# Optimization experiments

Measured on AMD Instinct MI355X. Metric: run time of the kernel, lower is better.

Reference implementation:

```python
import jax, jax.numpy as jnp
import numpy as np

N_NODES = 100000
N_EDGES = 800000
IN_FEATS = 64
H_FEATS = 64
INTER = 64
NUM_CLASSES = 32
NEG_SLOPE = 0.01  # torch leaky_relu default


def setup_inputs() -> dict:
    key = jax.random.key(0)
    ks = jax.random.split(key, 16)
    inp = {
        "gate_type": jax.random.randint(ks[0], (N_NODES,), 0, IN_FEATS),
        "src": jax.random.randint(ks[1], (N_EDGES,), 0, N_NODES),
        "dst": jax.random.randint(ks[2], (N_EDGES,), 0, N_NODES),
        "src_idx": jax.random.uniform(ks[3], (N_EDGES,), dtype=jnp.float32),
        "dst_idx": jax.random.uniform(ks[4], (N_EDGES,), dtype=jnp.float32),
        "rev": jax.random.uniform(ks[5], (N_EDGES,), dtype=jnp.float32),
        "emb": jax.random.normal(ks[6], (IN_FEATS, IN_FEATS), dtype=jnp.float32) * 0.1,
        # 5 stacked QConv layers (in_feats == h_feats so shapes coincide)
        "W1": jax.random.normal(ks[7], (5, INTER, IN_FEATS + 3), dtype=jnp.float32) * 0.1,
        "W2": jax.random.normal(ks[8], (5, H_FEATS, IN_FEATS + INTER), dtype=jnp.float32) * 0.1,
        "b2": jnp.zeros((5, H_FEATS), dtype=jnp.float32),
        "Wl1": jax.random.normal(ks[9], (H_FEATS, H_FEATS), dtype=jnp.float32) * 0.1,
        "bl1": jnp.zeros((H_FEATS,), dtype=jnp.float32),
        "Wl2": jax.random.normal(ks[10], (NUM_CLASSES, H_FEATS), dtype=jnp.float32) * 0.1,
        "bl2": jnp.zeros((NUM_CLASSES,), dtype=jnp.float32),
    }
    return inp


def _leaky_relu(x):
    return jnp.where(x >= 0, x, NEG_SLOPE * x)


def reference(gate_type, src, dst, src_idx, dst_idx, rev,
              emb, W1, W2, b2, Wl1, bl1, Wl2, bl2):
    n = gate_type.shape[0]
    # edge feature w: [E, 3]
    w = jnp.stack([src_idx, dst_idx, rev], axis=1)
    # in-degree for mailbox mean (zero-degree nodes get h_N = 0, as in DGL)
    deg = jax.ops.segment_sum(jnp.ones((src.shape[0],), w.dtype), dst, num_segments=n)
    inv_deg = (1.0 / jnp.maximum(deg, 1.0))[:, None]  # [N, 1]

    h = emb[gate_type]  # [N, F] embedding lookup
    for i in range(5):
        m = jnp.concatenate([h[src], w], axis=1)          # [E, F+3] gather
        tmp = _leaky_relu(m @ W1[i].T)                     # [E, inter]
        h_N = jax.ops.segment_sum(tmp, dst, num_segments=n) * inv_deg  # mean mailbox
        h = jax.nn.relu(jnp.concatenate([h, h_N], axis=1) @ W2[i].T + b2[i])
    h = jax.nn.relu(h @ Wl1.T + bl1)
    return h @ Wl2.T + bl2  # [N, num_classes]
```

## Files before the change

kernel.cpp:

```cpp
#include <hip/hip_runtime.h>

#define NN 100000
#define NE 800000
#define NBLK 391
#define NBUCK 196
#define EPB 3125
#define BCAP 6144

typedef __attribute__((ext_vector_type(8))) short short8;
typedef __attribute__((ext_vector_type(4))) float f32x4;

__device__ __forceinline__ unsigned short f2b(float x) {
  unsigned int u = __float_as_uint(x);
  u = u + 0x7fffu + ((u >> 16) & 1u);
  return (unsigned short)(u >> 16);
}
__device__ __forceinline__ float b2f(unsigned short s) {
  return __uint_as_float(((unsigned int)s) << 16);
}


__global__ __launch_bounds__(256) void ehist(const int* __restrict__ dst,
                                             int* __restrict__ hp) {
  __shared__ int lh[NBUCK];
  int tid = threadIdx.x;
  if (tid < NBUCK) lh[tid] = 0;
  __syncthreads();
  int e0 = blockIdx.x * EPB;
  for (int i = tid; i < EPB; i += 256) atomicAdd(&lh[dst[e0 + i] >> 9], 1);
  __syncthreads();
  if (tid < NBUCK) hp[blockIdx.x * NBUCK + tid] = lh[tid];
}

__global__ void escan(int* __restrict__ hp, int* __restrict__ bucket_start) {
  __shared__ int ws[4];
  int b = threadIdx.x;
  int running = 0;
  if (b < NBUCK) {
    for (int blk = 0; blk < 256; ++blk) {
      int t = hp[blk * NBUCK + b];
      hp[blk * NBUCK + b] = running;
      running += t;
    }
  }
  int lane = b & 63, wv = b >> 6;
  int v = running;
#pragma unroll
  for (int off = 1; off < 64; off <<= 1) {
    int t = __shfl_up(v, off);
    if (lane >= off) v += t;
  }
  if (lane == 63) ws[wv] = v;
  __syncthreads();
  int wpre = 0;
  for (int j = 0; j < wv; ++j) wpre += ws[j];
  int excl = v + wpre - running;
  if (b <= NBUCK) bucket_start[b] = excl;
}

__global__ __launch_bounds__(256) void escatter(
    const int* __restrict__ dst, const int* __restrict__ hp,
    const int* __restrict__ bucket_start, unsigned int* __restrict__ ebkt) {
  __shared__ int cur[NBUCK];
  int tid = threadIdx.x;
  if (tid < NBUCK) cur[tid] = bucket_start[tid] + hp[blockIdx.x * NBUCK + tid];
  __syncthreads();
  int e0 = blockIdx.x * EPB;
  for (int i = tid; i < EPB; i += 256) {
    int e = e0 + i;
    int d = dst[e];
    int pos = atomicAdd(&cur[d >> 9], 1);
    ebkt[pos] = ((unsigned int)(d & 511) << 20) | (unsigned int)e;
  }
}

__global__ __launch_bounds__(256) void bucket_csr(
    const unsigned int* __restrict__ ebkt, const int* __restrict__ bstart,
    const int* __restrict__ src, const float* __restrict__ si,
    const float* __restrict__ di, const float* __restrict__ rv,
    float4* __restrict__ erec, int* __restrict__ deg,
    float4* __restrict__ meta) {
  __shared__ unsigned int wbuf[BCAP];
  __shared__ int eidbuf[BCAP];
  __shared__ int cnt[512];
  __shared__ int excl[512];
  __shared__ int ws[4];
  int b = blockIdx.x, tid = threadIdx.x;
  int s0 = bstart[b];
  int size = bstart[b + 1] - s0;
  if (size > BCAP) size = BCAP;
  cnt[2 * tid] = 0;
  cnt[2 * tid + 1] = 0;
  for (int p = tid; p < size; p += 256) wbuf[p] = ebkt[s0 + p];
  __syncthreads();
  for (int p = tid; p < size; p += 256) atomicAdd(&cnt[wbuf[p] >> 20], 1);
  __syncthreads();
  int a = cnt[2 * tid], c = cnt[2 * tid + 1];
  int ps = a + c;
  int lane = tid & 63, wv = tid >> 6;
  int v = ps;
#pragma unroll
  for (int off = 1; off < 64; off <<= 1) {
    int t = __shfl_up(v, off);
    if (lane >= off) v += t;
  }
  if (lane == 63) ws[wv] = v;
  __syncthreads();
  int wpre = 0;
  for (int j = 0; j < wv; ++j) wpre += ws[j];
  int ex = v + wpre - ps;
  excl[2 * tid] = ex;
  excl[2 * tid + 1] = ex + a;
  int n0 = b << 9;
#pragma unroll
  for (int j = 0; j < 2; ++j) {
    int i = 2 * tid + j;
    int n = n0 + i;
    if (n < NN) {
      int d = j ? c : a;
      int rs = s0 + (j ? ex + a : ex);
      deg[n] = d;
      float4 m;
      m.x = __int_as_float(rs);
      m.y = __int_as_float(d);
      m.z = 1.0f / (float)((d > 1) ? d : 1);
      m.w = 0.f;
      meta[n] = m;
    }
  }
  cnt[2 * tid] = 0;
  cnt[2 * tid + 1] = 0;
  __syncthreads();
  for (int p = tid; p < size; p += 256) {
    unsigned int wd = wbuf[p];
    int ld = wd >> 20;
    int pos = excl[ld] + atomicAdd(&cnt[ld], 1);
    eidbuf[pos] = (int)(wd & 0xFFFFFu);
  }
  __syncthreads();
  for (int p = tid; p < size; p += 256) {
    int e = eidbuf[p];
    float4 r;
    r.x = __int_as_float(src[e]);
    r.y = si[e];
    r.z = di[e];
    r.w = rv[e];
    erec[s0 + p] = r;
  }
}


__global__ __launch_bounds__(256) void nhist(const int* __restrict__ deg,
                                             int* __restrict__ nhp) {
  __shared__ int lh[64];
  int tid = threadIdx.x;
  if (tid < 64) lh[tid] = 0;
  __syncthreads();
  int n = blockIdx.x * 256 + tid;
  if (n < NN) {
    int d = deg[n];
    atomicAdd(&lh[(d < 63) ? d : 63], 1);
  }
  __syncthreads();
  if (tid < 64) nhp[blockIdx.x * 64 + tid] = lh[tid];
}

__global__ void nscan(int* __restrict__ nhp, int* __restrict__ nbin_start) {
  int b = threadIdx.x;
  int running = 0;
  for (int blk = 0; blk < NBLK; ++blk) {
    int t = nhp[blk * 64 + b];
    nhp[blk * 64 + b] = running;
    running += t;
  }
  int v = running, s = running;
#pragma unroll
  for (int off = 1; off < 64; off <<= 1) {
    int t = __shfl_up(s, off);
    if (b >= off) s += t;
  }
  nbin_start[b] = s - v;
}

__global__ __launch_bounds__(256) void nscatter(const int* __restrict__ deg,
                                                const int* __restrict__ nhp,
                                                const int* __restrict__ nbin_start,
                                                int* __restrict__ order) {
  __shared__ int cur[64];
  int tid = threadIdx.x;
  if (tid < 64) cur[tid] = nbin_start[tid] + nhp[blockIdx.x * 64 + tid];
  __syncthreads();
  int n = blockIdx.x * 256 + tid;
  if (n < NN) {
    int d = deg[n];
    int pos = atomicAdd(&cur[(d < 63) ? d : 63], 1);
    order[pos] = n;
  }
}


__global__ __launch_bounds__(256) void aggregate(
    const unsigned short* __restrict__ H1, const float4* __restrict__ meta,
    const int* __restrict__ order, const float4* __restrict__ erec,
    const float* __restrict__ W1, unsigned short* __restrict__ hNs) {
  __shared__ float wcol[3][64];
  int tid = threadIdx.x;
  if (tid < 192) {
    int f = tid & 63, j = tid >> 6;
    wcol[j][f] = W1[f * 67 + 64 + j];
  }
  __syncthreads();
  int l = tid & 63;
  int fl = l & 15, f0 = fl * 4;
  int qidx = blockIdx.x * 16 + (tid >> 4);
  float wa[4], wb[4], wc[4];
#pragma unroll
  for (int j = 0; j < 4; ++j) {
    wa[j] = wcol[0][f0 + j];
    wb[j] = wcol[1][f0 + j];
    wc[j] = wcol[2][f0 + j];
  }
  if (qidx >= NN) return;
  int n = order[qidx];
  float4 m = meta[n];
  int s0 = __float_as_int(m.x);
  int cnt = __float_as_int(m.y);
  float invd = m.z;
  float acc[4] = {0.f, 0.f, 0.f, 0.f};
  float4 rc, rn;
  rc.x = rc.y = rc.z = rc.w = 0.f;
  rn.x = rn.y = rn.z = rn.w = 0.f;
  ushort4 hc = make_ushort4(0, 0, 0, 0);
  if (cnt > 0) {
    rc = erec[s0];
    hc = *(const ushort4*)&H1[(size_t)__float_as_int(rc.x) * 64 + f0];
    if (cnt > 1) rn = erec[s0 + 1];
  }
  for (int k = 0; k < cnt; ++k) {
    float4 rn2;
    rn2.x = rn2.y = rn2.z = rn2.w = 0.f;
    if (k + 2 < cnt) rn2 = erec[s0 + k + 2];
    ushort4 hn = make_ushort4(0, 0, 0, 0);
    if (k + 1 < cnt)
      hn = *(const ushort4*)&H1[(size_t)__float_as_int(rn.x) * 64 + f0];
    float hx[4] = {b2f(hc.x), b2f(hc.y), b2f(hc.z), b2f(hc.w)};
#pragma unroll
    for (int j = 0; j < 4; ++j) {
      float v = hx[j] + rc.y * wa[j] + rc.z * wb[j] + rc.w * wc[j];
      acc[j] += (v >= 0.f) ? v : 0.01f * v;
    }
    rc = rn;
    hc = hn;
    rn = rn2;
  }
  ushort4 o = make_ushort4(f2b(acc[0] * invd), f2b(acc[1] * invd),
                           f2b(acc[2] * invd), f2b(acc[3] * invd));
  *(ushort4*)&hNs[(size_t)n * 64 + f0] = o;
}


__device__ __forceinline__ void stageW(const float* W, int ws,
                                       unsigned short* lds, int CO, int K,
                                       int tid) {
  for (int idx = tid; idx < CO * K; idx += 256) {
    int c = idx / K, k = idx - c * K;
    int byte = (c * K + k) * 2;
    byte ^= ((c & 7) << 4);
    *(unsigned short*)((char*)lds + byte) = f2b(W[c * ws + k]);
  }
}
__device__ __forceinline__ short8 ldW(const unsigned short* lds, int K, int c,
                                      int k) {
  int byte = (c * K + k) * 2;
  byte ^= ((c & 7) << 4);
  return *(const short8*)((const char*)lds + byte);
}
__device__ __forceinline__ void stH(unsigned short* ht, int row, int col,
                                    unsigned short v) {
  int byte = row * 128 + col * 2;
  byte ^= ((row & 7) << 4);
  *(unsigned short*)((char*)ht + byte) = v;
}
__device__ __forceinline__ short8 ldH(const unsigned short* ht, int row,
                                      int k) {
  int byte = row * 128 + k * 2;
  byte ^= ((row & 7) << 4);
  return *(const short8*)((const char*)ht + byte);
}

__global__ __launch_bounds__(256) void fused0(
    const int* __restrict__ gate, const float* __restrict__ emb,
    const float* __restrict__ W1, unsigned short* __restrict__ hout,
    unsigned short* __restrict__ H1out) {
  __shared__ unsigned short W1l[64 * 64];
  int tid = threadIdx.x;
  stageW(W1, 67, W1l, 64, 64, tid);
  __syncthreads();
  int w = tid >> 6, l = tid & 63, r16 = l & 15, kg = l >> 4;
  int row_base = blockIdx.x * 128 + w * 32;
  f32x4 acc[2][4];
#pragma unroll
  for (int rt = 0; rt < 2; ++rt)
#pragma unroll
    for (int ct = 0; ct < 4; ++ct) {
      f32x4 z = {0.f, 0.f, 0.f, 0.f};
      acc[rt][ct] = z;
    }
#pragma unroll
  for (int rt = 0; rt < 2; ++rt) {
    int arow = row_base + rt * 16 + r16;
    short8 a0 = {0, 0, 0, 0, 0, 0, 0, 0};
    short8 a1 = {0, 0, 0, 0, 0, 0, 0, 0};
    if (arow < NN) {
      int g = gate[arow];
      const float* ep = &emb[g * 64];
      float4 e0 = *(const float4*)&ep[kg * 8];
      float4 e1 = *(const float4*)&ep[kg * 8 + 4];
      float4 e2 = *(const float4*)&ep[32 + kg * 8];
      float4 e3 = *(const float4*)&ep[32 + kg * 8 + 4];
      a0[0] = (short)f2b(e0.x); a0[1] = (short)f2b(e0.y);
      a0[2] = (short)f2b(e0.z); a0[3] = (short)f2b(e0.w);
      a0[4] = (short)f2b(e1.x); a0[5] = (short)f2b(e1.y);
      a0[6] = (short)f2b(e1.z); a0[7] = (short)f2b(e1.w);
      a1[0] = (short)f2b(e2.x); a1[1] = (short)f2b(e2.y);
      a1[2] = (short)f2b(e2.z); a1[3] = (short)f2b(e2.w);
      a1[4] = (short)f2b(e3.x); a1[5] = (short)f2b(e3.y);
      a1[6] = (short)f2b(e3.z); a1[7] = (short)f2b(e3.w);
      *(short8*)&hout[(size_t)arow * 64 + kg * 8] = a0;
      *(short8*)&hout[(size_t)arow * 64 + 32 + kg * 8] = a1;
    }
#pragma unroll
    for (int ct = 0; ct < 4; ++ct) {
      int c = ct * 16 + r16;
      acc[rt][ct] = __builtin_amdgcn_mfma_f32_16x16x32_bf16(
          a0, ldW(W1l, 64, c, kg * 8), acc[rt][ct], 0, 0, 0);
      acc[rt][ct] = __builtin_amdgcn_mfma_f32_16x16x32_bf16(
          a1, ldW(W1l, 64, c, 32 + kg * 8), acc[rt][ct], 0, 0, 0);
    }
  }
#pragma unroll
  for (int rt = 0; rt < 2; ++rt)
#pragma unroll
    for (int ct = 0; ct < 4; ++ct) {
      int col = ct * 16 + r16;
#pragma unroll
      for (int i = 0; i < 4; ++i) {
        int row = row_base + rt * 16 + kg * 4 + i;
        if (row < NN) H1out[(size_t)row * 64 + col] = f2b(acc[rt][ct][i]);
      }
    }
}

__global__ __launch_bounds__(256) void fused_mid(
    const unsigned short* h, const unsigned short* __restrict__ hNs,
    const float* __restrict__ W2, const float* __restrict__ b2,
    const float* __restrict__ W1n, unsigned short* hout,
    unsigned short* __restrict__ H1out) {
  __shared__ unsigned short W2l[64 * 128];
  __shared__ unsigned short W1l[64 * 64];
  __shared__ unsigned short ht[128 * 64];
  int tid = threadIdx.x;
  stageW(W2, 128, W2l, 64, 128, tid);
  stageW(W1n, 67, W1l, 64, 64, tid);
  __syncthreads();
  int w = tid >> 6, l = tid & 63, r16 = l & 15, kg = l >> 4;
  int row_base = blockIdx.x * 128 + w * 32;
  f32x4 acc[2][4];
#pragma unroll
  for (int rt = 0; rt < 2; ++rt)
#pragma unroll
    for (int ct = 0; ct < 4; ++ct) {
      f32x4 z = {0.f, 0.f, 0.f, 0.f};
      acc[rt][ct] = z;
    }
#pragma unroll
  for (int rt = 0; rt < 2; ++rt) {
    int arow = row_base + rt * 16 + r16;
    short8 a0 = {0, 0, 0, 0, 0, 0, 0, 0};
    short8 a1 = {0, 0, 0, 0, 0, 0, 0, 0};
    short8 c0 = {0, 0, 0, 0, 0, 0, 0, 0};
    short8 c1 = {0, 0, 0, 0, 0, 0, 0, 0};
    if (arow < NN) {
      a0 = *(const short8*)&h[(size_t)arow * 64 + kg * 8];
      a1 = *(const short8*)&h[(size_t)arow * 64 + 32 + kg * 8];
      c0 = *(const short8*)&hNs[(size_t)arow * 64 + kg * 8];
      c1 = *(const short8*)&hNs[(size_t)arow * 64 + 32 + kg * 8];
    }
#pragma unroll
    for (int ct = 0; ct < 4; ++ct) {
      int c = ct * 16 + r16;
      acc[rt][ct] = __builtin_amdgcn_mfma_f32_16x16x32_bf16(
          a0, ldW(W2l, 128, c, kg * 8), acc[rt][ct], 0, 0, 0);
      acc[rt][ct] = __builtin_amdgcn_mfma_f32_16x16x32_bf16(
          a1, ldW(W2l, 128, c, 32 + kg * 8), acc[rt][ct], 0, 0, 0);
      acc[rt][ct] = __builtin_amdgcn_mfma_f32_16x16x32_bf16(
          c0, ldW(W2l, 128, c, 64 + kg * 8), acc[rt][ct], 0, 0, 0);
      acc[rt][ct] = __builtin_amdgcn_mfma_f32_16x16x32_bf16(
          c1, ldW(W2l, 128, c, 96 + kg * 8), acc[rt][ct], 0, 0, 0);
    }
  }
#pragma unroll
  for (int rt = 0; rt < 2; ++rt)
#pragma unroll
    for (int ct = 0; ct < 4; ++ct) {
      int col = ct * 16 + r16;
      float bv = b2[col];
#pragma unroll
      for (int i = 0; i < 4; ++i) {
        int lrow = w * 32 + rt * 16 + kg * 4 + i;
        float v = acc[rt][ct][i] + bv;
        v = fmaxf(v, 0.f);
        stH(ht, lrow, col, f2b(v));
      }
    }
  __syncthreads();
  f32x4 acc2[2][4];
#pragma unroll
  for (int rt = 0; rt < 2; ++rt)
#pragma unroll
    for (int ct = 0; ct < 4; ++ct) {
      f32x4 z = {0.f, 0.f, 0.f, 0.f};
      acc2[rt][ct] = z;
    }
#pragma unroll
  for (int rt = 0; rt < 2; ++rt) {
    int lrow = w * 32 + rt * 16 + r16;
    int arow = row_base + rt * 16 + r16;
    short8 a0 = ldH(ht, lrow, kg * 8);
    short8 a1 = ldH(ht, lrow, 32 + kg * 8);
    if (arow < NN) {
      *(short8*)&hout[(size_t)arow * 64 + kg * 8] = a0;
      *(short8*)&hout[(size_t)arow * 64 + 32 + kg * 8] = a1;
    }
#pragma unroll
    for (int ct = 0; ct < 4; ++ct) {
      int c = ct * 16 + r16;
      acc2[rt][ct] = __builtin_amdgcn_mfma_f32_16x16x32_bf16(
          a0, ldW(W1l, 64, c, kg * 8), acc2[rt][ct], 0, 0, 0);
      acc2[rt][ct] = __builtin_amdgcn_mfma_f32_16x16x32_bf16(
          a1, ldW(W1l, 64, c, 32 + kg * 8), acc2[rt][ct], 0, 0, 0);
    }
  }
#pragma unroll
  for (int rt = 0; rt < 2; ++rt)
#pragma unroll
    for (int ct = 0; ct < 4; ++ct) {
      int col = ct * 16 + r16;
#pragma unroll
      for (int i = 0; i < 4; ++i) {
        int row = row_base + rt * 16 + kg * 4 + i;
        if (row < NN) H1out[(size_t)row * 64 + col] = f2b(acc2[rt][ct][i]);
      }
    }
}

__global__ __launch_bounds__(256) void fused_final(
    const unsigned short* __restrict__ h, const unsigned short* __restrict__ hNs,
    const float* __restrict__ W2, const float* __restrict__ b2,
    const float* __restrict__ Wl1, const float* __restrict__ bl1,
    const float* __restrict__ Wl2, const float* __restrict__ bl2,
    float* __restrict__ out) {
  __shared__ unsigned short W2l[64 * 128];
  __shared__ unsigned short Al[64 * 64];
  __shared__ unsigned short Bl[32 * 64];
  __shared__ unsigned short ht[128 * 64];
  int tid = threadIdx.x;
  stageW(W2, 128, W2l, 64, 128, tid);
  stageW(Wl1, 64, Al, 64, 64, tid);
  stageW(Wl2, 64, Bl, 32, 64, tid);
  __syncthreads();
  int w = tid >> 6, l = tid & 63, r16 = l & 15, kg = l >> 4;
  int row_base = blockIdx.x * 128 + w * 32;
  f32x4 acc[2][4];
#pragma unroll
  for (int rt = 0; rt < 2; ++rt)
#pragma unroll
    for (int ct = 0; ct < 4; ++ct) {
      f32x4 z = {0.f, 0.f, 0.f, 0.f};
      acc[rt][ct] = z;
    }
#pragma unroll
  for (int rt = 0; rt < 2; ++rt) {
    int arow = row_base + rt * 16 + r16;
    short8 a0 = {0, 0, 0, 0, 0, 0, 0, 0};
    short8 a1 = {0, 0, 0, 0, 0, 0, 0, 0};
    short8 c0 = {0, 0, 0, 0, 0, 0, 0, 0};
    short8 c1 = {0, 0, 0, 0, 0, 0, 0, 0};
    if (arow < NN) {
      a0 = *(const short8*)&h[(size_t)arow * 64 + kg * 8];
      a1 = *(const short8*)&h[(size_t)arow * 64 + 32 + kg * 8];
      c0 = *(const short8*)&hNs[(size_t)arow * 64 + kg * 8];
      c1 = *(const short8*)&hNs[(size_t)arow * 64 + 32 + kg * 8];
    }
#pragma unroll
    for (int ct = 0; ct < 4; ++ct) {
      int c = ct * 16 + r16;
      acc[rt][ct] = __builtin_amdgcn_mfma_f32_16x16x32_bf16(
          a0, ldW(W2l, 128, c, kg * 8), acc[rt][ct], 0, 0, 0);
      acc[rt][ct] = __builtin_amdgcn_mfma_f32_16x16x32_bf16(
          a1, ldW(W2l, 128, c, 32 + kg * 8), acc[rt][ct], 0, 0, 0);
      acc[rt][ct] = __builtin_amdgcn_mfma_f32_16x16x32_bf16(
          c0, ldW(W2l, 128, c, 64 + kg * 8), acc[rt][ct], 0, 0, 0);
      acc[rt][ct] = __builtin_amdgcn_mfma_f32_16x16x32_bf16(
          c1, ldW(W2l, 128, c, 96 + kg * 8), acc[rt][ct], 0, 0, 0);
    }
  }
#pragma unroll
  for (int rt = 0; rt < 2; ++rt)
#pragma unroll
    for (int ct = 0; ct < 4; ++ct) {
      int col = ct * 16 + r16;
      float bv = b2[col];
#pragma unroll
      for (int i = 0; i < 4; ++i) {
        int lrow = w * 32 + rt * 16 + kg * 4 + i;
        float v = acc[rt][ct][i] + bv;
        v = fmaxf(v, 0.f);
        stH(ht, lrow, col, f2b(v));
      }
    }
  __syncthreads();
  f32x4 acc2[2][4];
#pragma unroll
  for (int rt = 0; rt < 2; ++rt)
#pragma unroll
    for (int ct = 0; ct < 4; ++ct) {
      f32x4 z = {0.f, 0.f, 0.f, 0.f};
      acc2[rt][ct] = z;
    }
#pragma unroll
  for (int rt = 0; rt < 2; ++rt) {
    int lrow = w * 32 + rt * 16 + r16;
    short8 a0 = ldH(ht, lrow, kg * 8);
    short8 a1 = ldH(ht, lrow, 32 + kg * 8);
#pragma unroll
    for (int ct = 0; ct < 4; ++ct) {
      int c = ct * 16 + r16;
      acc2[rt][ct] = __builtin_amdgcn_mfma_f32_16x16x32_bf16(
          a0, ldW(Al, 64, c, kg * 8), acc2[rt][ct], 0, 0, 0);
      acc2[rt][ct] = __builtin_amdgcn_mfma_f32_16x16x32_bf16(
          a1, ldW(Al, 64, c, 32 + kg * 8), acc2[rt][ct], 0, 0, 0);
    }
  }
  __syncthreads();
#pragma unroll
  for (int rt = 0; rt < 2; ++rt)
#pragma unroll
    for (int ct = 0; ct < 4; ++ct) {
      int col = ct * 16 + r16;
      float bv = bl1[col];
#pragma unroll
      for (int i = 0; i < 4; ++i) {
        int lrow = w * 32 + rt * 16 + kg * 4 + i;
        float v = acc2[rt][ct][i] + bv;
        v = fmaxf(v, 0.f);
        stH(ht, lrow, col, f2b(v));
      }
    }
  __syncthreads();
  f32x4 acc3[2][2];
#pragma unroll
  for (int rt = 0; rt < 2; ++rt)
#pragma unroll
    for (int ct = 0; ct < 2; ++ct) {
      f32x4 z = {0.f, 0.f, 0.f, 0.f};
      acc3[rt][ct] = z;
    }
#pragma unroll
  for (int rt = 0; rt < 2; ++rt) {
    int lrow = w * 32 + rt * 16 + r16;
    short8 a0 = ldH(ht, lrow, kg * 8);
    short8 a1 = ldH(ht, lrow, 32 + kg * 8);
#pragma unroll
    for (int ct = 0; ct < 2; ++ct) {
      int c = ct * 16 + r16;
      acc3[rt][ct] = __builtin_amdgcn_mfma_f32_16x16x32_bf16(
          a0, ldW(Bl, 64, c, kg * 8), acc3[rt][ct], 0, 0, 0);
      acc3[rt][ct] = __builtin_amdgcn_mfma_f32_16x16x32_bf16(
          a1, ldW(Bl, 64, c, 32 + kg * 8), acc3[rt][ct], 0, 0, 0);
    }
  }
#pragma unroll
  for (int rt = 0; rt < 2; ++rt)
#pragma unroll
    for (int ct = 0; ct < 2; ++ct) {
      int col = ct * 16 + r16;
      float bv = bl2[col];
#pragma unroll
      for (int i = 0; i < 4; ++i) {
        int row = row_base + rt * 16 + kg * 4 + i;
        if (row < NN) out[(size_t)row * 32 + col] = acc3[rt][ct][i] + bv;
      }
    }
}


extern "C" void kernel_launch(void* const* d_in, const int* in_sizes, int n_in,
                              void* d_out, int out_size, void* d_ws, size_t ws_size,
                              hipStream_t stream) {
  const int* gate = (const int*)d_in[0];
  const int* src = (const int*)d_in[1];
  const int* dst = (const int*)d_in[2];
  const float* src_idx = (const float*)d_in[3];
  const float* dst_idx = (const float*)d_in[4];
  const float* rev = (const float*)d_in[5];
  const float* emb = (const float*)d_in[6];
  const float* W1 = (const float*)d_in[7];
  const float* W2 = (const float*)d_in[8];
  const float* b2 = (const float*)d_in[9];
  const float* Wl1 = (const float*)d_in[10];
  const float* bl1 = (const float*)d_in[11];
  const float* Wl2 = (const float*)d_in[12];
  const float* bl2 = (const float*)d_in[13];
  float* out = (float*)d_out;

  char* ws = (char*)d_ws;
  unsigned short* h = (unsigned short*)(ws + 0);
  unsigned short* H1 = (unsigned short*)(ws + 12800000);
  unsigned short* hNs = (unsigned short*)(ws + 25600000);
  float4* erec = (float4*)(ws + 38400000);
  unsigned int* ebkt = (unsigned int*)(ws + 51200000);
  float4* meta = (float4*)(ws + 54400000);
  int* order = (int*)(ws + 56000000);
  int* deg = (int*)(ws + 56400000);
  int* hist_part = (int*)(ws + 56800000);
  int* bucket_start = (int*)(ws + 57000960);
  int* nhist_part = (int*)(ws + 57002000);
  int* nbin_start = (int*)(ws + 57102096);

  ehist<<<256, 256, 0, stream>>>(dst, hist_part);
  escan<<<1, 256, 0, stream>>>(hist_part, bucket_start);
  escatter<<<256, 256, 0, stream>>>(dst, hist_part, bucket_start, ebkt);
  bucket_csr<<<NBUCK, 256, 0, stream>>>(ebkt, bucket_start, src, src_idx,
                                        dst_idx, rev, erec, deg, meta);
  nhist<<<NBLK, 256, 0, stream>>>(deg, nhist_part);
  nscan<<<1, 64, 0, stream>>>(nhist_part, nbin_start);
  nscatter<<<NBLK, 256, 0, stream>>>(deg, nhist_part, nbin_start, order);

  fused0<<<782, 256, 0, stream>>>(gate, emb, W1, h, H1);
  for (int i = 0; i < 5; ++i) {
    aggregate<<<6250, 256, 0, stream>>>(H1, meta, order,
                                        erec, W1 + i * 64 * 67, hNs);
    if (i < 4)
      fused_mid<<<782, 256, 0, stream>>>(h, hNs, W2 + i * 64 * 128, b2 + i * 64,
                                         W1 + (i + 1) * 64 * 67, h, H1);
  }
  fused_final<<<782, 256, 0, stream>>>(h, hNs, W2 + 4 * 64 * 128, b2 + 4 * 64,
                                       Wl1, bl1, Wl2, bl2, out);
}
```

Before: 431.1 us.

## Move edge-record gather into bucket scatter, fold degree histogram, deepen aggregate prefetch

The bucket scatter now writes full edge records (src and the three edge features) plus a 16-bit local destination id directly in bucket order. The CSR kernel then only permutes records within a bucket instead of doing a random gather by edge id. The node-degree histogram is folded into the CSR kernel, which removes the separate nhist launch, and nscatter now handles 512 nodes per block to match the bucket granularity. The aggregate loop prefetches the edge record three ahead and the H1 row two ahead instead of two and one. This adds register pressure, and the scratch buffers are aliased onto the h and hNs regions, which are only safe because they are consumed before fused0 and aggregate write those regions.

Result: faster. 397.3 us (-7.8%).

```diff
diff --git a/kernel.cpp b/kernel.cpp
--- a/kernel.cpp
+++ b/kernel.cpp
@@ -2,7 +2,6 @@
 
 #define NN 100000
 #define NE 800000
-#define NBLK 391
 #define NBUCK 196
 #define EPB 3125
 #define BCAP 6144
@@ -33,7 +32,7 @@
 }
 
 __global__ void escan(int* __restrict__ hp, int* __restrict__ bucket_start) {
-  __shared__ int ws[4];
+  __shared__ int wsum[4];
   int b = threadIdx.x;
   int running = 0;
   if (b < NBUCK) {
@@ -50,17 +49,20 @@
     int t = __shfl_up(v, off);
     if (lane >= off) v += t;
   }
-  if (lane == 63) ws[wv] = v;
+  if (lane == 63) wsum[wv] = v;
   __syncthreads();
   int wpre = 0;
-  for (int j = 0; j < wv; ++j) wpre += ws[j];
+  for (int j = 0; j < wv; ++j) wpre += wsum[j];
   int excl = v + wpre - running;
   if (b <= NBUCK) bucket_start[b] = excl;
 }
 
 __global__ __launch_bounds__(256) void escatter(
-    const int* __restrict__ dst, const int* __restrict__ hp,
-    const int* __restrict__ bucket_start, unsigned int* __restrict__ ebkt) {
+    const int* __restrict__ dst, const int* __restrict__ src,
+    const float* __restrict__ si, const float* __restrict__ di,
+    const float* __restrict__ rv, const int* __restrict__ hp,
+    const int* __restrict__ bucket_start, float4* __restrict__ erec_tmp,
+    unsigned short* __restrict__ lbkt) {
   __shared__ int cur[NBUCK];
   int tid = threadIdx.x;
   if (tid < NBUCK) cur[tid] = bucket_start[tid] + hp[blockIdx.x * NBUCK + tid];
@@ -70,30 +72,38 @@
     int e = e0 + i;
     int d = dst[e];
     int pos = atomicAdd(&cur[d >> 9], 1);
-    ebkt[pos] = ((unsigned int)(d & 511) << 20) | (unsigned int)e;
+    float4 r;
+    r.x = __int_as_float(src[e]);
+    r.y = si[e];
+    r.z = di[e];
+    r.w = rv[e];
+    erec_tmp[pos] = r;
+    lbkt[pos] = (unsigned short)(d & 511);
   }
 }
 
 __global__ __launch_bounds__(256) void bucket_csr(
-    const unsigned int* __restrict__ ebkt, const int* __restrict__ bstart,
-    const int* __restrict__ src, const float* __restrict__ si,
-    const float* __restrict__ di, const float* __restrict__ rv,
-    float4* __restrict__ erec, int* __restrict__ deg,
-    float4* __restrict__ meta) {
-  __shared__ unsigned int wbuf[BCAP];
-  __shared__ int eidbuf[BCAP];
+    const unsigned short* __restrict__ lbkt, const int* __restrict__ bstart,
+    const float4* __restrict__ erec_tmp, float4* __restrict__ erec,
+    int* __restrict__ deg, float4* __restrict__ meta, int* __restrict__ nhp) {
+  __shared__ unsigned short lb[BCAP];
   __shared__ int cnt[512];
   __shared__ int excl[512];
-  __shared__ int ws[4];
+  __shared__ int dh[64];
+  __shared__ int wsum[4];
   int b = blockIdx.x, tid = threadIdx.x;
   int s0 = bstart[b];
   int size = bstart[b + 1] - s0;
   if (size > BCAP) size = BCAP;
   cnt[2 * tid] = 0;
   cnt[2 * tid + 1] = 0;
-  for (int p = tid; p < size; p += 256) wbuf[p] = ebkt[s0 + p];
-  __syncthreads();
-  for (int p = tid; p < size; p += 256) atomicAdd(&cnt[wbuf[p] >> 20], 1);
+  if (tid < 64) dh[tid] = 0;
+  __syncthreads();
+  for (int p = tid; p < size; p += 256) {
+    unsigned short v = lbkt[s0 + p];
+    lb[p] = v;
+    atomicAdd(&cnt[v], 1);
+  }
   __syncthreads();
   int a = cnt[2 * tid], c = cnt[2 * tid + 1];
   int ps = a + c;
@@ -104,10 +114,10 @@
     int t = __shfl_up(v, off);
     if (lane >= off) v += t;
   }
-  if (lane == 63) ws[wv] = v;
+  if (lane == 63) wsum[wv] = v;
   __syncthreads();
   int wpre = 0;
-  for (int j = 0; j < wv; ++j) wpre += ws[j];
+  for (int j = 0; j < wv; ++j) wpre += wsum[j];
   int ex = v + wpre - ps;
   excl[2 * tid] = ex;
   excl[2 * tid + 1] = ex + a;
@@ -126,49 +136,25 @@
       m.z = 1.0f / (float)((d > 1) ? d : 1);
       m.w = 0.f;
       meta[n] = m;
+      atomicAdd(&dh[(d < 63) ? d : 63], 1);
     }
   }
   cnt[2 * tid] = 0;
   cnt[2 * tid + 1] = 0;
   __syncthreads();
   for (int p = tid; p < size; p += 256) {
-    unsigned int wd = wbuf[p];
-    int ld = wd >> 20;
+    int ld = lb[p];
     int pos = excl[ld] + atomicAdd(&cnt[ld], 1);
-    eidbuf[pos] = (int)(wd & 0xFFFFFu);
-  }
-  __syncthreads();
-  for (int p = tid; p < size; p += 256) {
-    int e = eidbuf[p];
-    float4 r;
-    r.x = __int_as_float(src[e]);
-    r.y = si[e];
-    r.z = di[e];
-    r.w = rv[e];
-    erec[s0 + p] = r;
-  }
-}
-
-
-__global__ __launch_bounds__(256) void nhist(const int* __restrict__ deg,
-                                             int* __restrict__ nhp) {
-  __shared__ int lh[64];
-  int tid = threadIdx.x;
-  if (tid < 64) lh[tid] = 0;
-  __syncthreads();
-  int n = blockIdx.x * 256 + tid;
-  if (n < NN) {
-    int d = deg[n];
-    atomicAdd(&lh[(d < 63) ? d : 63], 1);
-  }
-  __syncthreads();
-  if (tid < 64) nhp[blockIdx.x * 64 + tid] = lh[tid];
-}
+    erec[s0 + pos] = erec_tmp[s0 + p];
+  }
+  if (tid < 64) nhp[b * 64 + tid] = dh[tid];
+}
+
 
 __global__ void nscan(int* __restrict__ nhp, int* __restrict__ nbin_start) {
   int b = threadIdx.x;
   int running = 0;
-  for (int blk = 0; blk < NBLK; ++blk) {
+  for (int blk = 0; blk < NBUCK; ++blk) {
     int t = nhp[blk * 64 + b];
     nhp[blk * 64 + b] = running;
     running += t;
@@ -182,19 +168,22 @@
   nbin_start[b] = s - v;
 }
 
-__global__ __launch_bounds__(256) void nscatter(const int* __restrict__ deg,
-                                                const int* __restrict__ nhp,
-                                                const int* __restrict__ nbin_start,
-                                                int* __restrict__ order) {
+__global__ __launch_bounds__(256) void nscatter(
+    const int* __restrict__ deg, const int* __restrict__ nhp,
+    const int* __restrict__ nbin_start, int* __restrict__ order) {
   __shared__ int cur[64];
   int tid = threadIdx.x;
   if (tid < 64) cur[tid] = nbin_start[tid] + nhp[blockIdx.x * 64 + tid];
   __syncthreads();
-  int n = blockIdx.x * 256 + tid;
-  if (n < NN) {
-    int d = deg[n];
-    int pos = atomicAdd(&cur[(d < 63) ? d : 63], 1);
-    order[pos] = n;
+  int n0 = blockIdx.x * 512;
+#pragma unroll
+  for (int j = 0; j < 2; ++j) {
+    int n = n0 + tid + j * 256;
+    if (n < NN) {
+      int d = deg[n];
+      int pos = atomicAdd(&cur[(d < 63) ? d : 63], 1);
+      order[pos] = n;
+    }
   }
 }
 
@@ -227,31 +216,38 @@
   int cnt = __float_as_int(m.y);
   float invd = m.z;
   float acc[4] = {0.f, 0.f, 0.f, 0.f};
-  float4 rc, rn;
-  rc.x = rc.y = rc.z = rc.w = 0.f;
-  rn.x = rn.y = rn.z = rn.w = 0.f;
-  ushort4 hc = make_ushort4(0, 0, 0, 0);
+  float4 r0, r1, r2;
+  r0.x = r0.y = r0.z = r0.w = 0.f;
+  r1 = r0;
+  r2 = r0;
+  ushort4 h0 = make_ushort4(0, 0, 0, 0), h1 = h0;
   if (cnt > 0) {
-    rc = erec[s0];
-    hc = *(const ushort4*)&H1[(size_t)__float_as_int(rc.x) * 64 + f0];
-    if (cnt > 1) rn = erec[s0 + 1];
-  }
+    r0 = erec[s0];
+    h0 = *(const ushort4*)&H1[(size_t)__float_as_int(r0.x) * 64 + f0];
+  }
+  if (cnt > 1) {
+    r1 = erec[s0 + 1];
+    h1 = *(const ushort4*)&H1[(size_t)__float_as_int(r1.x) * 64 + f0];
+  }
+  if (cnt > 2) r2 = erec[s0 + 2];
   for (int k = 0; k < cnt; ++k) {
-    float4 rn2;
-    rn2.x = rn2.y = rn2.z = rn2.w = 0.f;
-    if (k + 2 < cnt) rn2 = erec[s0 + k + 2];
-    ushort4 hn = make_ushort4(0, 0, 0, 0);
-    if (k + 1 < cnt)
-      hn = *(const ushort4*)&H1[(size_t)__float_as_int(rn.x) * 64 + f0];
-    float hx[4] = {b2f(hc.x), b2f(hc.y), b2f(hc.z), b2f(hc.w)};
+    float4 r3;
+    r3.x = r3.y = r3.z = r3.w = 0.f;
+    if (k + 3 < cnt) r3 = erec[s0 + k + 3];
+    ushort4 h2 = make_ushort4(0, 0, 0, 0);
+    if (k + 2 < cnt)
+      h2 = *(const ushort4*)&H1[(size_t)__float_as_int(r2.x) * 64 + f0];
+    float hx[4] = {b2f(h0.x), b2f(h0.y), b2f(h0.z), b2f(h0.w)};
 #pragma unroll
     for (int j = 0; j < 4; ++j) {
-      float v = hx[j] + rc.y * wa[j] + rc.z * wb[j] + rc.w * wc[j];
-      acc[j] += (v >= 0.f) ? v : 0.01f * v;
-    }
-    rc = rn;
-    hc = hn;
-    rn = rn2;
+      float vv = hx[j] + r0.y * wa[j] + r0.z * wb[j] + r0.w * wc[j];
+      acc[j] += (vv >= 0.f) ? vv : 0.01f * vv;
+    }
+    r0 = r1;
+    r1 = r2;
+    r2 = r3;
+    h0 = h1;
+    h1 = h2;
   }
   ushort4 o = make_ushort4(f2b(acc[0] * invd), f2b(acc[1] * invd),
                            f2b(acc[2] * invd), f2b(acc[3] * invd));
@@ -616,26 +612,27 @@
 
   char* ws = (char*)d_ws;
   unsigned short* h = (unsigned short*)(ws + 0);
+  unsigned short* lbkt = (unsigned short*)(ws + 0);
   unsigned short* H1 = (unsigned short*)(ws + 12800000);
   unsigned short* hNs = (unsigned short*)(ws + 25600000);
+  float4* erec_tmp = (float4*)(ws + 25600000);
   float4* erec = (float4*)(ws + 38400000);
-  unsigned int* ebkt = (unsigned int*)(ws + 51200000);
-  float4* meta = (float4*)(ws + 54400000);
-  int* order = (int*)(ws + 56000000);
-  int* deg = (int*)(ws + 56400000);
-  int* hist_part = (int*)(ws + 56800000);
-  int* bucket_start = (int*)(ws + 57000960);
-  int* nhist_part = (int*)(ws + 57002000);
-  int* nbin_start = (int*)(ws + 57102096);
+  float4* meta = (float4*)(ws + 51200000);
+  int* order = (int*)(ws + 52800000);
+  int* deg = (int*)(ws + 53200000);
+  int* hist_part = (int*)(ws + 53600000);
+  int* bucket_start = (int*)(ws + 53810000);
+  int* nhp = (int*)(ws + 53820000);
+  int* nbin_start = (int*)(ws + 53880000);
 
   ehist<<<256, 256, 0, stream>>>(dst, hist_part);
   escan<<<1, 256, 0, stream>>>(hist_part, bucket_start);
-  escatter<<<256, 256, 0, stream>>>(dst, hist_part, bucket_start, ebkt);
-  bucket_csr<<<NBUCK, 256, 0, stream>>>(ebkt, bucket_start, src, src_idx,
-                                        dst_idx, rev, erec, deg, meta);
-  nhist<<<NBLK, 256, 0, stream>>>(deg, nhist_part);
-  nscan<<<1, 64, 0, stream>>>(nhist_part, nbin_start);
-  nscatter<<<NBLK, 256, 0, stream>>>(deg, nhist_part, nbin_start, order);
+  escatter<<<256, 256, 0, stream>>>(dst, src, src_idx, dst_idx, rev, hist_part,
+                                    bucket_start, erec_tmp, lbkt);
+  bucket_csr<<<NBUCK, 256, 0, stream>>>(lbkt, bucket_start, erec_tmp, erec,
+                                        deg, meta, nhp);
+  nscan<<<1, 64, 0, stream>>>(nhp, nbin_start);
+  nscatter<<<NBUCK, 256, 0, stream>>>(deg, nhp, nbin_start, order);
 
   fused0<<<782, 256, 0, stream>>>(gate, emb, W1, h, H1);
   for (int i = 0; i < 5; ++i) {
```
